# Kernel tuning notes

Hardware: AMD Instinct MI355X
Metric: run time of the kernel (lower is better)

Reference implementation:

```python
import jax, jax.numpy as jnp
import numpy as np

B, S, D, H = 4, 2048, 1024, 16
HD = D // H  # head_size = 64
SCALE = HD ** -0.5


def setup_inputs() -> dict:
    key = jax.random.key(0)
    k1, k2, k3 = jax.random.split(key, 3)
    hidden_states = jax.random.normal(k1, (B, S, D), dtype=jnp.float32)
    W_qkv = jax.random.normal(k2, (D, 3 * D), dtype=jnp.float32) * 0.02
    W_out = jax.random.normal(k3, (D, D), dtype=jnp.float32) * 0.02
    return {"hidden_states": hidden_states, "W_qkv": W_qkv, "W_out": W_out}


def reference(hidden_states, W_qkv, W_out):
    b, s, d = hidden_states.shape
    qkv = hidden_states @ W_qkv                      # [b, s, 3d]
    q, k, v = jnp.split(qkv, 3, axis=-1)
    # [b, s, d] -> [b, H, s, hd]
    q = q.reshape(b, s, H, HD).transpose(0, 2, 1, 3)
    k = k.reshape(b, s, H, HD).transpose(0, 2, 1, 3)
    v = v.reshape(b, s, H, HD).transpose(0, 2, 1, 3)
    scores = jnp.einsum("bhqd,bhkd->bhqk", q, k) * SCALE  # [b, H, s, s]
    probs = jax.nn.softmax(scores, axis=-1)
    ctx = jnp.einsum("bhqk,bhkd->bhqd", probs, v)         # [b, H, s, hd]
    ctx = ctx.transpose(0, 2, 1, 3).reshape(b, s, d)
    out = ctx @ W_out
    return out
```

## Files before the change

### kernel.cpp

```cpp
#include <hip/hip_runtime.h>

typedef __attribute__((ext_vector_type(8))) __bf16 bf8;
typedef __attribute__((ext_vector_type(4))) float f4;
typedef __attribute__((ext_vector_type(8))) unsigned short us8;
typedef __attribute__((ext_vector_type(4))) unsigned short us4;
typedef __attribute__((ext_vector_type(4))) unsigned int u32x4;
typedef __attribute__((ext_vector_type(2))) unsigned int u32x2;

#define MFMA16(a, b, c) __builtin_amdgcn_mfma_f32_16x16x32_bf16((a), (b), (c), 0, 0, 0)
#define GLOAD16(gp, lp)                                                        \
  __builtin_amdgcn_global_load_lds(                                            \
      (const __attribute__((address_space(1))) void*)(gp),                     \
      (__attribute__((address_space(3))) void*)(lp), 16, 0, 0)

__device__ __forceinline__ unsigned short f2bf(float f) {
  unsigned u = __builtin_bit_cast(unsigned, f);
  u += 0x7FFFu + ((u >> 16) & 1u);
  return (unsigned short)(u >> 16);
}

__device__ __forceinline__ float fexp2(float x) {
  float r;
  asm("v_exp_f32 %0, %1" : "=v"(r) : "v"(x));
  return r;
}

__device__ __forceinline__ unsigned cvtpk(float a, float b) {
  unsigned r;
  asm("v_cvt_pk_bf16_f32 %0, %1, %2" : "=v"(r) : "v"(a), "v"(b));
  return r;
}

__global__ __launch_bounds__(256) void c_prep(const float* __restrict__ hs,
                                              unsigned short* __restrict__ hsb,
                                              const float* __restrict__ wqkv,
                                              unsigned short* __restrict__ wqt,
                                              const float* __restrict__ wout,
                                              unsigned short* __restrict__ wot) {
  __shared__ float T[64][65];
  const int bid = blockIdx.x;
  const int t = threadIdx.x;
  if (bid < 4096) {
    int i = bid * 256 + t;
    const float4* p = reinterpret_cast<const float4*>(hs) + (size_t)i * 2;
    float4 a = p[0], b = p[1];
    us8 o;
    o[0] = f2bf(a.x); o[1] = f2bf(a.y); o[2] = f2bf(a.z); o[3] = f2bf(a.w);
    o[4] = f2bf(b.x); o[5] = f2bf(b.y); o[6] = f2bf(b.z); o[7] = f2bf(b.w);
    *reinterpret_cast<us8*>(&hsb[(size_t)i * 8]) = o;
    return;
  }
  const float* in;
  unsigned short* out;
  int R = 1024, C, idx;
  if (bid < 4864) { idx = bid - 4096; in = wqkv; out = wqt; C = 3072; }
  else            { idx = bid - 4864; in = wout; out = wot; C = 1024; }
  const int nbc = C >> 6;
  const int c0 = (idx % nbc) * 64, r0 = (idx / nbc) * 64;
  const int tr = t >> 4, tc = (t & 15) * 4;
#pragma unroll
  for (int i = 0; i < 4; ++i) {
    int r = tr + i * 16;
    float4 v = *reinterpret_cast<const float4*>(&in[(size_t)(r0 + r) * C + c0 + tc]);
    T[r][tc] = v.x; T[r][tc + 1] = v.y; T[r][tc + 2] = v.z; T[r][tc + 3] = v.w;
  }
  __syncthreads();
#pragma unroll
  for (int i = 0; i < 4; ++i) {
    int c = tr + i * 16;
    us4 o;
    o[0] = f2bf(T[tc + 0][c]); o[1] = f2bf(T[tc + 1][c]);
    o[2] = f2bf(T[tc + 2][c]); o[3] = f2bf(T[tc + 3][c]);
    *reinterpret_cast<us4*>(&out[(size_t)(c0 + c) * R + r0 + tc]) = o;
  }
}

__global__ __launch_bounds__(256) void k_qkv(const unsigned short* __restrict__ A,
                                             const unsigned short* __restrict__ Bt,
                                             unsigned short* __restrict__ Qo,
                                             unsigned short* __restrict__ Ko,
                                             unsigned short* __restrict__ Vo) {
  __shared__ unsigned short As[2][128 * 32];
  __shared__ unsigned short Bs[2][128 * 32];
  const int t = threadIdx.x;
  const int lane = t & 63, wid = t >> 6;
  const int wr = wid >> 1, wc = wid & 1;
  const int cl = lane & 15, kr8 = (lane >> 4) << 3;
  const int id = blockIdx.x;
  const int s = (id & 7) * 192 + (id >> 3);
  const int m0 = (s / 24) << 7, n0 = (s % 24) << 7;

  f4 acc[4][4];
#pragma unroll
  for (int i = 0; i < 4; ++i)
#pragma unroll
    for (int j = 0; j < 4; ++j) acc[i][j] = (f4){0.f, 0.f, 0.f, 0.f};

  auto STAGE = [&](int buf, int kt) {
    int k0 = kt << 5;
#pragma unroll
    for (int it = 0; it < 2; ++it) {
      int c = t + (it << 8);
      int wb = (t & 192) + (it << 8);
      GLOAD16(A + (size_t)(m0 + (c >> 2)) * 1024 + k0 + ((c & 3) << 3),
              (char*)As[buf] + (size_t)wb * 16);
      GLOAD16(Bt + (size_t)(n0 + (c >> 2)) * 1024 + k0 + ((c & 3) << 3),
              (char*)Bs[buf] + (size_t)wb * 16);
    }
  };

  STAGE(0, 0);
  __syncthreads();
  for (int kt = 0; kt < 32; ++kt) {
    int cur = kt & 1;
    if (kt < 31) STAGE(cur ^ 1, kt + 1);
    const unsigned short* as = As[cur];
    const unsigned short* bs = Bs[cur];
    bf8 af[4], bfr[4];
#pragma unroll
    for (int mi = 0; mi < 4; ++mi)
      af[mi] = *reinterpret_cast<const bf8*>(&as[(wr * 64 + mi * 16 + cl) * 32 + kr8]);
#pragma unroll
    for (int ni = 0; ni < 4; ++ni)
      bfr[ni] = *reinterpret_cast<const bf8*>(&bs[(wc * 64 + ni * 16 + cl) * 32 + kr8]);
#pragma unroll
    for (int mi = 0; mi < 4; ++mi)
#pragma unroll
      for (int ni = 0; ni < 4; ++ni)
        acc[mi][ni] = MFMA16(af[mi], bfr[ni], acc[mi][ni]);
    __syncthreads();
  }

#pragma unroll
  for (int mi = 0; mi < 4; ++mi) {
#pragma unroll
    for (int ni = 0; ni < 4; ++ni) {
      int gcol = n0 + wc * 64 + ni * 16 + cl;
      int grow0 = m0 + wr * 64 + mi * 16 + ((lane >> 4) << 2);
      int b = grow0 >> 11, s0 = grow0 & 2047;
      if (gcol < 1024) {
        int h = gcol >> 6, hd = gcol & 63;
#pragma unroll
        for (int r = 0; r < 4; ++r)
          Qo[((size_t)(b * 16 + h) * 2048 + s0 + r) * 64 + hd] =
              f2bf(acc[mi][ni][r] * 0.18033688011112042f);
      } else if (gcol < 2048) {
        int cc = gcol - 1024;
        int h = cc >> 6, hd = cc & 63;
#pragma unroll
        for (int r = 0; r < 4; ++r)
          Ko[((size_t)(b * 16 + h) * 2048 + s0 + r) * 64 + hd] = f2bf(acc[mi][ni][r]);
      } else {
        int cc = gcol - 2048;
        int h = cc >> 6, hd = cc & 63;
        us4 o;
        o[0] = f2bf(acc[mi][ni][0]); o[1] = f2bf(acc[mi][ni][1]);
        o[2] = f2bf(acc[mi][ni][2]); o[3] = f2bf(acc[mi][ni][3]);
        *reinterpret_cast<us4*>(&Vo[((size_t)(b * 16 + h) * 64 + hd) * 2048 + s0]) = o;
      }
    }
  }
}

__global__ __launch_bounds__(512) void k_attn(const unsigned short* __restrict__ Q,
                                              const unsigned short* __restrict__ K,
                                              const unsigned short* __restrict__ Vt,
                                              unsigned short* __restrict__ Ctx) {
  __shared__ __align__(16) unsigned short SMEM[4][2][64 * 64];
  __shared__ float RedS[128];
  const int t = threadIdx.x;
  const int lane = t & 63, wid = t >> 6;
  const int cl = lane & 15, g = lane >> 4;
  const int qg = wid >> 1, kg = wid & 1;
  const int id = blockIdx.x;
  const int sw = (id & 7) * 128 + (id >> 3);
  const int bh = sw >> 4, qb = sw & 15;
  const int b = bh >> 4, h = bh & 15;
  const int q0 = qb << 7;
  const size_t base = (size_t)bh * (2048 * 64);

  bf8 qf[2][2];
#pragma unroll
  for (int qi = 0; qi < 2; ++qi) {
    int qrow = q0 + qg * 32 + qi * 16 + cl;
    qf[qi][0] = *reinterpret_cast<const bf8*>(&Q[base + (size_t)qrow * 64 + (g << 3)]);
    qf[qi][1] = *reinterpret_cast<const bf8*>(&Q[base + (size_t)qrow * 64 + 32 + (g << 3)]);
  }

  const unsigned ones_u = 0x3F803F80u;
  u32x4 ones4 = (u32x4){ones_u, ones_u, ones_u, ones_u};
  bf8 onesb = __builtin_bit_cast(bf8, ones4);
  const f4 minit = (f4){-12.f, -12.f, -12.f, -12.f};

  f4 o[2][4], osum[2];
#pragma unroll
  for (int qi = 0; qi < 2; ++qi) {
#pragma unroll
    for (int n = 0; n < 4; ++n) o[qi][n] = (f4){0.f, 0.f, 0.f, 0.f};
    osum[qi] = (f4){0.f, 0.f, 0.f, 0.f};
  }

  auto STAGEK = [&](int slot, int kv0) {
    int kvl = t >> 3;
    int dblk = (t & 7) ^ (kvl & 7);
    GLOAD16(K + base + (size_t)(kv0 + kvl) * 64 + (dblk << 3),
            (char*)SMEM[slot][0] + (size_t)(t & 448) * 16);
  };
  auto STAGEV = [&](int slot, int kv0) {
    int d = t >> 3, ch = t & 7;
    int kq = ch ^ ((d >> 1) & 7);
    GLOAD16(Vt + base + (size_t)d * 2048 + kv0 + (kq << 3),
            (char*)SMEM[slot][1] + (size_t)(t & 448) * 16);
  };

  auto COMPUTE = [&](const char* kp, const char* vp) {
    f4 sT[2][2];
    __builtin_amdgcn_s_setprio(1);
#pragma unroll
    for (int cb = 0; cb < 2; ++cb) {
      int row = (2 * kg + cb) * 16 + cl;
      bf8 a0 = *reinterpret_cast<const bf8*>(kp + row * 128 + ((g ^ (cl & 7)) << 4));
      bf8 a1 = *reinterpret_cast<const bf8*>(kp + row * 128 + (((4 + g) ^ (cl & 7)) << 4));
#pragma unroll
      for (int qi = 0; qi < 2; ++qi) {
        f4 s = minit;
        s = MFMA16(a0, qf[qi][0], s);
        s = MFMA16(a1, qf[qi][1], s);
        sT[cb][qi] = s;
      }
    }
    __builtin_amdgcn_s_setprio(0);

    u32x4 pw[2];
#pragma unroll
    for (int qi = 0; qi < 2; ++qi) {
      pw[qi][0] = cvtpk(fexp2(sT[0][qi][0]), fexp2(sT[0][qi][1]));
      pw[qi][1] = cvtpk(fexp2(sT[0][qi][2]), fexp2(sT[0][qi][3]));
      pw[qi][2] = cvtpk(fexp2(sT[1][qi][0]), fexp2(sT[1][qi][1]));
      pw[qi][3] = cvtpk(fexp2(sT[1][qi][2]), fexp2(sT[1][qi][3]));
    }
    bf8 pa0 = __builtin_bit_cast(bf8, pw[0]);
    bf8 pa1 = __builtin_bit_cast(bf8, pw[1]);

    const int q1 = 8 * kg + g, q2 = 8 * kg + 4 + g;
    unsigned vb = (unsigned)(cl * 128);
    unsigned o1 = (unsigned)((q1 ^ (cl & 14)) << 3);
    unsigned o2 = (unsigned)((q2 ^ (cl & 14)) << 3);
    __builtin_amdgcn_s_setprio(1);
#pragma unroll
    for (int n = 0; n < 4; ++n) {
      unsigned a = vb + (unsigned)(n * 2048);
      u32x2 lo = *reinterpret_cast<const u32x2*>(vp + a + o1);
      u32x2 hi = *reinterpret_cast<const u32x2*>(vp + a + o2);
      u32x4 bw = (u32x4){lo[0], lo[1], hi[0], hi[1]};
      bf8 vb8 = __builtin_bit_cast(bf8, bw);
      o[0][n] = MFMA16(pa0, vb8, o[0][n]);
      o[1][n] = MFMA16(pa1, vb8, o[1][n]);
    }
    osum[0] = MFMA16(pa0, onesb, osum[0]);
    osum[1] = MFMA16(pa1, onesb, osum[1]);
    __builtin_amdgcn_s_setprio(0);
  };

  STAGEK(0, 0);
  STAGEV(0, 0);
  STAGEK(1, 64);
  STAGEV(1, 64);
  __syncthreads();

  for (int ti = 0; ti < 16; ++ti) {
    int t0 = 2 * ti, t1 = t0 + 1;
    if (ti < 15) {
      STAGEK((t0 + 2) & 3, (t0 + 2) << 6);
      STAGEV((t0 + 2) & 3, (t0 + 2) << 6);
      STAGEK((t1 + 2) & 3, (t1 + 2) << 6);
      STAGEV((t1 + 2) & 3, (t1 + 2) << 6);
    }
    COMPUTE((const char*)SMEM[t0 & 3][0], (const char*)SMEM[t0 & 3][1]);
    COMPUTE((const char*)SMEM[t1 & 3][0], (const char*)SMEM[t1 & 3][1]);
    __syncthreads();
  }

  float* red = (float*)SMEM;
  if (kg) {
#pragma unroll
    for (int qi = 0; qi < 2; ++qi) {
#pragma unroll
      for (int n = 0; n < 4; ++n) {
        int ridx = qg * 8 + qi * 4 + n;
        *reinterpret_cast<f4*>(red + ridx * 256 + cl * 16 + g * 4) = o[qi][n];
      }
      if (cl == 0)
        *reinterpret_cast<f4*>(&RedS[(qg * 2 + qi) * 16 + g * 4]) = osum[qi];
    }
  }
  __syncthreads();
  if (!kg) {
#pragma unroll
    for (int qi = 0; qi < 2; ++qi) {
#pragma unroll
      for (int n = 0; n < 4; ++n) {
        int ridx = qg * 8 + qi * 4 + n;
        f4 po = *reinterpret_cast<const f4*>(red + ridx * 256 + cl * 16 + g * 4);
        o[qi][n] += po;
      }
      f4 ps = *reinterpret_cast<const f4*>(&RedS[(qg * 2 + qi) * 16 + g * 4]);
      osum[qi] += ps;
#pragma unroll
      for (int r = 0; r < 4; ++r) {
        float inv = 1.0f / osum[qi][r];
        int s = q0 + qg * 32 + qi * 16 + (g << 2) + r;
        size_t rb = ((size_t)b * 2048 + s) * 1024 + h * 64;
#pragma unroll
        for (int n = 0; n < 4; ++n) Ctx[rb + n * 16 + cl] = f2bf(o[qi][n][r] * inv);
      }
    }
  }
}

__global__ __launch_bounds__(256) void k_oproj(const unsigned short* __restrict__ A,
                                               const unsigned short* __restrict__ Bt,
                                               float* __restrict__ Out) {
  __shared__ unsigned short As[2][128 * 32];
  __shared__ unsigned short Bs[2][128 * 32];
  const int t = threadIdx.x;
  const int lane = t & 63, wid = t >> 6;
  const int wr = wid >> 1, wc = wid & 1;
  const int cl = lane & 15, kr8 = (lane >> 4) << 3;
  const int id = blockIdx.x;
  const int s = (id & 7) * 64 + (id >> 3);
  const int m0 = (s >> 3) << 7, n0 = (s & 7) << 7;

  f4 acc[4][4];
#pragma unroll
  for (int i = 0; i < 4; ++i)
#pragma unroll
    for (int j = 0; j < 4; ++j) acc[i][j] = (f4){0.f, 0.f, 0.f, 0.f};

  auto STAGE = [&](int buf, int kt) {
    int k0 = kt << 5;
#pragma unroll
    for (int it = 0; it < 2; ++it) {
      int c = t + (it << 8);
      int wb = (t & 192) + (it << 8);
      GLOAD16(A + (size_t)(m0 + (c >> 2)) * 1024 + k0 + ((c & 3) << 3),
              (char*)As[buf] + (size_t)wb * 16);
      GLOAD16(Bt + (size_t)(n0 + (c >> 2)) * 1024 + k0 + ((c & 3) << 3),
              (char*)Bs[buf] + (size_t)wb * 16);
    }
  };

  STAGE(0, 0);
  __syncthreads();
  for (int kt = 0; kt < 32; ++kt) {
    int cur = kt & 1;
    if (kt < 31) STAGE(cur ^ 1, kt + 1);
    const unsigned short* as = As[cur];
    const unsigned short* bs = Bs[cur];
    bf8 af[4], bfr[4];
#pragma unroll
    for (int mi = 0; mi < 4; ++mi)
      af[mi] = *reinterpret_cast<const bf8*>(&as[(wr * 64 + mi * 16 + cl) * 32 + kr8]);
#pragma unroll
    for (int ni = 0; ni < 4; ++ni)
      bfr[ni] = *reinterpret_cast<const bf8*>(&bs[(wc * 64 + ni * 16 + cl) * 32 + kr8]);
#pragma unroll
    for (int mi = 0; mi < 4; ++mi)
#pragma unroll
      for (int ni = 0; ni < 4; ++ni)
        acc[mi][ni] = MFMA16(af[mi], bfr[ni], acc[mi][ni]);
    __syncthreads();
  }

#pragma unroll
  for (int mi = 0; mi < 4; ++mi) {
#pragma unroll
    for (int ni = 0; ni < 4; ++ni) {
      int gcol = n0 + wc * 64 + ni * 16 + cl;
#pragma unroll
      for (int r = 0; r < 4; ++r) {
        int grow = m0 + wr * 64 + mi * 16 + ((lane >> 4) << 2) + r;
        Out[(size_t)grow * 1024 + gcol] = acc[mi][ni][r];
      }
    }
  }
}

extern "C" void kernel_launch(void* const* d_in, const int* in_sizes, int n_in,
                              void* d_out, int out_size, void* d_ws, size_t ws_size,
                              hipStream_t stream) {
  const float* hs = (const float*)d_in[0];
  const float* wqkv = (const float*)d_in[1];
  const float* wout = (const float*)d_in[2];
  float* out = (float*)d_out;

  unsigned short* ws = (unsigned short*)d_ws;
  const size_t NHS = (size_t)8192 * 1024;
  const size_t NWQ = (size_t)1024 * 3072;
  const size_t NWO = (size_t)1024 * 1024;
  const size_t NQ = (size_t)64 * 2048 * 64;

  unsigned short* hsb = ws;
  unsigned short* wqt = ws + NHS;
  unsigned short* wot = wqt + NWQ;
  unsigned short* Qw = wot + NWO;
  unsigned short* Kw = Qw + NQ;
  unsigned short* Vw = Kw + NQ;
  unsigned short* Cw = hsb;

  c_prep<<<dim3(5120), 256, 0, stream>>>(hs, hsb, wqkv, wqt, wout, wot);
  k_qkv<<<dim3(1536), 256, 0, stream>>>(hsb, wqt, Qw, Kw, Vw);
  k_attn<<<dim3(1024), 512, 0, stream>>>(Qw, Kw, Vw, Cw);
  k_oproj<<<dim3(512), 256, 0, stream>>>(Cw, wot, out);
}
```

Before: 186.7 us.

## Rewrite QKV GEMM with 256x256 tiles, 8 waves, swizzled LDS and K=64 steps

The QKV projection GEMM moves from 128x128 tiles with 4 waves and K=32 steps to 256x256 tiles with 8 waves and K=64 steps. LDS is XOR-swizzled to avoid bank conflicts, and the loop adds sub-step barriers plus s_setprio around MFMA bursts. The aim is more operand reuse per byte loaded, fewer global loads, and fewer LDS conflicts. In exchange the grid shrinks to 384 blocks, which may leave some CUs underused, and register pressure rises with 32 accumulators per thread.

```diff
diff --git a/kernel.cpp b/kernel.cpp
--- a/kernel.cpp
+++ b/kernel.cpp
@@ -75,88 +75,118 @@
   }
 }
 
-__global__ __launch_bounds__(256) void k_qkv(const unsigned short* __restrict__ A,
-                                             const unsigned short* __restrict__ Bt,
-                                             unsigned short* __restrict__ Qo,
-                                             unsigned short* __restrict__ Ko,
-                                             unsigned short* __restrict__ Vo) {
-  __shared__ unsigned short As[2][128 * 32];
-  __shared__ unsigned short Bs[2][128 * 32];
+__global__ __launch_bounds__(512, 2) void k_qkv8(const unsigned short* __restrict__ A,
+                                                 const unsigned short* __restrict__ Bt,
+                                                 unsigned short* __restrict__ Qo,
+                                                 unsigned short* __restrict__ Ko,
+                                                 unsigned short* __restrict__ Vo) {
+  __shared__ __align__(16) unsigned short Asl[2][2][128 * 64];
+  __shared__ __align__(16) unsigned short Bsl[2][2][128 * 64];
   const int t = threadIdx.x;
   const int lane = t & 63, wid = t >> 6;
-  const int wr = wid >> 1, wc = wid & 1;
-  const int cl = lane & 15, kr8 = (lane >> 4) << 3;
+  const int cl = lane & 15, g = lane >> 4;
+  const int wm = wid >> 2, wn = wid & 3;
   const int id = blockIdx.x;
-  const int s = (id & 7) * 192 + (id >> 3);
-  const int m0 = (s / 24) << 7, n0 = (s % 24) << 7;
-
-  f4 acc[4][4];
-#pragma unroll
-  for (int i = 0; i < 4; ++i)
+  const int s = (id & 7) * 48 + (id >> 3);
+  const int mt = s / 12, ntile = s % 12;
+  const int m0 = mt << 8, n0 = ntile << 8;
+
+  f4 acc[8][4];
+#pragma unroll
+  for (int i = 0; i < 8; ++i)
 #pragma unroll
     for (int j = 0; j < 4; ++j) acc[i][j] = (f4){0.f, 0.f, 0.f, 0.f};
 
-  auto STAGE = [&](int buf, int kt) {
-    int k0 = kt << 5;
-#pragma unroll
-    for (int it = 0; it < 2; ++it) {
-      int c = t + (it << 8);
-      int wb = (t & 192) + (it << 8);
-      GLOAD16(A + (size_t)(m0 + (c >> 2)) * 1024 + k0 + ((c & 3) << 3),
-              (char*)As[buf] + (size_t)wb * 16);
-      GLOAD16(Bt + (size_t)(n0 + (c >> 2)) * 1024 + k0 + ((c & 3) << 3),
-              (char*)Bs[buf] + (size_t)wb * 16);
-    }
+  auto STAGE_TILE = [&](int kt) {
+    int slot = kt & 1;
+    size_t koff = (size_t)kt << 6;
+#pragma unroll
+    for (int hf = 0; hf < 2; ++hf)
+#pragma unroll
+      for (int it = 0; it < 2; ++it) {
+        int c = t + (it << 9);
+        int row = c >> 3;
+        int kb = (c & 7) ^ (row & 7);
+        int wb = (wid * 64 + (it << 9)) * 16;
+        GLOAD16(A + (size_t)(m0 + hf * 128 + row) * 1024 + koff + (kb << 3),
+                (char*)Asl[slot][hf] + wb);
+        GLOAD16(Bt + (size_t)(n0 + hf * 128 + row) * 1024 + koff + (kb << 3),
+                (char*)Bsl[slot][hf] + wb);
+      }
   };
 
-  STAGE(0, 0);
-  __syncthreads();
-  for (int kt = 0; kt < 32; ++kt) {
-    int cur = kt & 1;
-    if (kt < 31) STAGE(cur ^ 1, kt + 1);
-    const unsigned short* as = As[cur];
-    const unsigned short* bs = Bs[cur];
-    bf8 af[4], bfr[4];
-#pragma unroll
-    for (int mi = 0; mi < 4; ++mi)
-      af[mi] = *reinterpret_cast<const bf8*>(&as[(wr * 64 + mi * 16 + cl) * 32 + kr8]);
-#pragma unroll
-    for (int ni = 0; ni < 4; ++ni)
-      bfr[ni] = *reinterpret_cast<const bf8*>(&bs[(wc * 64 + ni * 16 + cl) * 32 + kr8]);
-#pragma unroll
-    for (int mi = 0; mi < 4; ++mi)
-#pragma unroll
-      for (int ni = 0; ni < 4; ++ni)
-        acc[mi][ni] = MFMA16(af[mi], bfr[ni], acc[mi][ni]);
-    __syncthreads();
-  }
-
-#pragma unroll
-  for (int mi = 0; mi < 4; ++mi) {
-#pragma unroll
-    for (int ni = 0; ni < 4; ++ni) {
-      int gcol = n0 + wc * 64 + ni * 16 + cl;
-      int grow0 = m0 + wr * 64 + mi * 16 + ((lane >> 4) << 2);
-      int b = grow0 >> 11, s0 = grow0 & 2047;
-      if (gcol < 1024) {
+  STAGE_TILE(0);
+  asm volatile("s_waitcnt vmcnt(0)" ::: "memory");
+  __builtin_amdgcn_s_barrier();
+
+  for (int kt = 0; kt < 16; ++kt) {
+    const int slot = kt & 1;
+    if (kt < 15) STAGE_TILE(kt + 1);
+    const char* ap = (const char*)Asl[slot][wm];
+    const char* bp = (const char*)Bsl[slot][wn >> 1];
+    bf8 af[4][2];
+#pragma unroll
+    for (int p4 = 0; p4 < 4; ++p4) {
+      const int qa = p4 >> 1, qb = p4 & 1;
+      if (qb == 0) {
+#pragma unroll
+        for (int mi = 0; mi < 4; ++mi) {
+          int ra = qa * 64 + mi * 16 + cl;
+          af[mi][0] = *reinterpret_cast<const bf8*>(ap + ra * 128 + ((g ^ (cl & 7)) << 4));
+          af[mi][1] = *reinterpret_cast<const bf8*>(ap + ra * 128 + (((4 + g) ^ (cl & 7)) << 4));
+        }
+      }
+      bf8 bfr[2][2];
+#pragma unroll
+      for (int ni = 0; ni < 2; ++ni) {
+        int rb = (wn & 1) * 64 + (qb * 2 + ni) * 16 + cl;
+        bfr[ni][0] = *reinterpret_cast<const bf8*>(bp + rb * 128 + ((g ^ (cl & 7)) << 4));
+        bfr[ni][1] = *reinterpret_cast<const bf8*>(bp + rb * 128 + (((4 + g) ^ (cl & 7)) << 4));
+      }
+      __builtin_amdgcn_s_barrier();
+      __builtin_amdgcn_s_setprio(1);
+#pragma unroll
+      for (int mi = 0; mi < 4; ++mi)
+#pragma unroll
+        for (int ni = 0; ni < 2; ++ni) {
+          acc[qa * 4 + mi][qb * 2 + ni] =
+              MFMA16(af[mi][0], bfr[ni][0], acc[qa * 4 + mi][qb * 2 + ni]);
+          acc[qa * 4 + mi][qb * 2 + ni] =
+              MFMA16(af[mi][1], bfr[ni][1], acc[qa * 4 + mi][qb * 2 + ni]);
+        }
+      __builtin_amdgcn_s_setprio(0);
+      if (p4 < 3) __builtin_amdgcn_s_barrier();
+    }
+    asm volatile("s_waitcnt vmcnt(0)" ::: "memory");
+    __builtin_amdgcn_s_barrier();
+  }
+
+  const float QSC = 0.18033688011112042f;
+#pragma unroll
+  for (int am = 0; am < 8; ++am) {
+    int grow0 = m0 + wm * 128 + am * 16 + g * 4;
+    int b = grow0 >> 11, s0 = grow0 & 2047;
+#pragma unroll
+    for (int an = 0; an < 4; ++an) {
+      int gcol = n0 + wn * 64 + an * 16 + cl;
+      if (ntile < 4) {
         int h = gcol >> 6, hd = gcol & 63;
-#pragma unroll
-        for (int r = 0; r < 4; ++r)
-          Qo[((size_t)(b * 16 + h) * 2048 + s0 + r) * 64 + hd] =
-              f2bf(acc[mi][ni][r] * 0.18033688011112042f);
-      } else if (gcol < 2048) {
+        size_t rb = ((size_t)(b * 16 + h) * 2048 + s0) * 64 + hd;
+#pragma unroll
+        for (int r = 0; r < 4; ++r) Qo[rb + (size_t)r * 64] = f2bf(acc[am][an][r] * QSC);
+      } else if (ntile < 8) {
         int cc = gcol - 1024;
         int h = cc >> 6, hd = cc & 63;
-#pragma unroll
-        for (int r = 0; r < 4; ++r)
-          Ko[((size_t)(b * 16 + h) * 2048 + s0 + r) * 64 + hd] = f2bf(acc[mi][ni][r]);
+        size_t rb = ((size_t)(b * 16 + h) * 2048 + s0) * 64 + hd;
+#pragma unroll
+        for (int r = 0; r < 4; ++r) Ko[rb + (size_t)r * 64] = f2bf(acc[am][an][r]);
       } else {
         int cc = gcol - 2048;
         int h = cc >> 6, hd = cc & 63;
-        us4 o;
-        o[0] = f2bf(acc[mi][ni][0]); o[1] = f2bf(acc[mi][ni][1]);
-        o[2] = f2bf(acc[mi][ni][2]); o[3] = f2bf(acc[mi][ni][3]);
-        *reinterpret_cast<us4*>(&Vo[((size_t)(b * 16 + h) * 64 + hd) * 2048 + s0]) = o;
+        us4 o4;
+        o4[0] = f2bf(acc[am][an][0]); o4[1] = f2bf(acc[am][an][1]);
+        o4[2] = f2bf(acc[am][an][2]); o4[3] = f2bf(acc[am][an][3]);
+        *reinterpret_cast<us4*>(&Vo[((size_t)(b * 16 + h) * 64 + hd) * 2048 + s0]) = o4;
       }
     }
   }
@@ -309,8 +339,8 @@
 #pragma unroll
       for (int r = 0; r < 4; ++r) {
         float inv = 1.0f / osum[qi][r];
-        int s = q0 + qg * 32 + qi * 16 + (g << 2) + r;
-        size_t rb = ((size_t)b * 2048 + s) * 1024 + h * 64;
+        int sq = q0 + qg * 32 + qi * 16 + (g << 2) + r;
+        size_t rb = ((size_t)b * 2048 + sq) * 1024 + h * 64;
 #pragma unroll
         for (int n = 0; n < 4; ++n) Ctx[rb + n * 16 + cl] = f2bf(o[qi][n][r] * inv);
       }
@@ -409,7 +439,7 @@
   unsigned short* Cw = hsb;
 
   c_prep<<<dim3(5120), 256, 0, stream>>>(hs, hsb, wqkv, wqt, wout, wot);
-  k_qkv<<<dim3(1536), 256, 0, stream>>>(hsb, wqt, Qw, Kw, Vw);
+  k_qkv8<<<dim3(384), 512, 0, stream>>>(hsb, wqt, Qw, Kw, Vw);
   k_attn<<<dim3(1024), 512, 0, stream>>>(Qw, Kw, Vw, Cw);
   k_oproj<<<dim3(512), 256, 0, stream>>>(Cw, wot, out);
 }
```

Result: slower. 199.5 us (+6.8%).
